# Performance work log

Hardware: AMD Instinct MI355X
Metric: run time of the kernel (lower is better)

## Reference

```python
import jax, jax.numpy as jnp
import numpy as np

HEADS = 8
DIM_HEAD = 64
SCALE = DIM_HEAD ** -0.5


def setup_inputs() -> dict:
    key = jax.random.key(0)
    k1, k2, k3, k4 = jax.random.split(key, 4)
    b, n, dim = 4, 1024, 512
    inner = HEADS * DIM_HEAD  # 512
    x = jax.random.normal(k1, (b, n, dim), dtype=jnp.float32)
    spd = jax.random.normal(k2, (b, HEADS, n, n), dtype=jnp.float32)
    head_keep = jnp.ones((HEADS,), dtype=jnp.float32)  # deterministic stand-in for binomial head drop
    w_qkv = jax.random.normal(k3, (dim, 3 * inner), dtype=jnp.float32) * (dim ** -0.5)
    w_out = jax.random.normal(k4, (inner, dim), dtype=jnp.float32) * (inner ** -0.5)
    b_out = jnp.zeros((dim,), dtype=jnp.float32)
    return {"x": x, "spd": spd, "head_keep": head_keep, "w_qkv": w_qkv, "w_out": w_out, "b_out": b_out}


def reference(x, spd, head_keep, w_qkv, w_out, b_out):
    b, n, dim = x.shape
    qkv = x @ w_qkv  # [b, n, 3*inner]
    q, k, v = jnp.split(qkv, 3, axis=-1)

    def to_heads(t):  # [b, n, h*d] -> [b, h, n, d]
        return t.reshape(b, n, HEADS, DIM_HEAD).transpose(0, 2, 1, 3)

    q, k, v = to_heads(q), to_heads(k), to_heads(v)
    dots = jnp.einsum('bhid,bhjd->bhij', q, k) * SCALE + spd  # [b, h, n, n]
    attn = jax.nn.softmax(dots, axis=-1)
    # random head drop + rescale: attn * mask * H / sum(keep)
    keep_sum = jnp.sum(head_keep)
    attn = attn * (head_keep[None, :, None, None] * (HEADS / keep_sum))
    out = jnp.einsum('bhij,bhjd->bhid', attn, v)  # [b, h, n, d]
    out = out.transpose(0, 2, 1, 3).reshape(b, n, HEADS * DIM_HEAD)
    return out @ w_out + b_out
```

## Files before the change

### kernel.cpp

```cpp
#include <hip/hip_runtime.h>
#include <math.h>

#define NSEQ   1024
#define HEADS  8
#define DHEAD  64
#define SCALE  0.125f
#define LOG2E  1.4426950408889634f

typedef unsigned int u32;
typedef unsigned short u16;
typedef short short8 __attribute__((ext_vector_type(8)));
typedef __bf16 bf16x2 __attribute__((ext_vector_type(2)));
typedef __bf16 bf16x8 __attribute__((ext_vector_type(8)));
typedef float f32x4  __attribute__((ext_vector_type(4)));
typedef float f32x16 __attribute__((ext_vector_type(16)));

__device__ __forceinline__ u16 f2bf(float f) {
    __bf16 h = (__bf16)f;
    return __builtin_bit_cast(u16, h);
}
__device__ __forceinline__ u32 pk2(float lo, float hi) {
    bf16x2 v; v[0] = (__bf16)lo; v[1] = (__bf16)hi;
    return __builtin_bit_cast(u32, v);
}
__device__ __forceinline__ float exp2_fast(float x) {
#if __has_builtin(__builtin_amdgcn_exp2f)
    return __builtin_amdgcn_exp2f(x);
#else
    return exp2f(x);
#endif
}
__device__ __forceinline__ f32x4 mfma16(short8 a, short8 b, f32x4 c) {
    return __builtin_amdgcn_mfma_f32_16x16x32_bf16(a, b, c, 0, 0, 0);
}
__device__ __forceinline__ f32x16 mfma32(short8 a, short8 b, f32x16 c) {
    return __builtin_amdgcn_mfma_f32_32x32x16_bf16(a, b, c, 0, 0, 0);
}

__global__ __launch_bounds__(256) void prep(const float* __restrict__ x,
                                            const float* __restrict__ wqkv,
                                            const float* __restrict__ wout,
                                            u16* __restrict__ x_bf,
                                            u16* __restrict__ wqkvT,
                                            u16* __restrict__ woutT) {
    __shared__ float T[64][65];
    const int t = threadIdx.x;
    const int bb = blockIdx.x;
    if (bb < 1024) {
        int i = (bb * 256 + t) * 8;
        float4 a = *(const float4*)&x[i];
        float4 b = *(const float4*)&x[i + 4];
        bf16x8 v;
        v[0] = (__bf16)a.x; v[1] = (__bf16)a.y; v[2] = (__bf16)a.z; v[3] = (__bf16)a.w;
        v[4] = (__bf16)b.x; v[5] = (__bf16)b.y; v[6] = (__bf16)b.z; v[7] = (__bf16)b.w;
        *(short8*)&x_bf[i] = __builtin_bit_cast(short8, v);
        return;
    }
    const float* in; u16* outp; int K, N, n0, k0;
    if (bb < 1216) {
        int bid = bb - 1024;
        in = wqkv; outp = wqkvT; K = 512; N = 1536;
        n0 = (bid % 24) * 64; k0 = (bid / 24) * 64;
    } else {
        int bid = bb - 1216;
        in = wout; outp = woutT; K = 512; N = 512;
        n0 = (bid % 8) * 64; k0 = (bid / 8) * 64;
    }
    #pragma unroll
    for (int rep = 0; rep < 4; ++rep) {
        int r = rep * 16 + (t >> 4), c = (t & 15) * 4;
        float4 v = *(const float4*)&in[(size_t)(k0 + r) * N + n0 + c];
        T[r][c + 0] = v.x; T[r][c + 1] = v.y; T[r][c + 2] = v.z; T[r][c + 3] = v.w;
    }
    __syncthreads();
    const int nl = t >> 2, kb = (t & 3) * 16;
    bf16x8 s0, s1;
    #pragma unroll
    for (int e = 0; e < 8; ++e) s0[e] = (__bf16)T[kb + e][nl];
    #pragma unroll
    for (int e = 0; e < 8; ++e) s1[e] = (__bf16)T[kb + 8 + e][nl];
    *(short8*)&outp[(size_t)(n0 + nl) * K + k0 + kb]     = __builtin_bit_cast(short8, s0);
    *(short8*)&outp[(size_t)(n0 + nl) * K + k0 + kb + 8] = __builtin_bit_cast(short8, s1);
}

__global__ __launch_bounds__(256) void gemm_qkv_mfma(const u16* __restrict__ xb,
                                                     const u16* __restrict__ wT,
                                                     u16* __restrict__ qb,
                                                     u16* __restrict__ kb,
                                                     u16* __restrict__ vT) {
    __shared__ u16 As[128][40];
    __shared__ u16 Bs[64][40];
    const int t = threadIdx.x, lane = t & 63, w = t >> 6;
    const int wm = w >> 1, wn = w & 1;
    const int l15 = lane & 15, l4 = lane >> 4;
    const int j0 = blockIdx.x * 64, i0 = blockIdx.y * 128;
    const int which = j0 / 512;
    const int b = i0 >> 10;

    f32x4 acc[8];
    #pragma unroll
    for (int i = 0; i < 8; ++i) acc[i] = (f32x4){0.f, 0.f, 0.f, 0.f};

    short8 ra[2], rbv;
    #pragma unroll
    for (int rep = 0; rep < 2; ++rep) {
        int row = rep * 64 + (t >> 2), c8 = (t & 3) * 8;
        ra[rep] = *(const short8*)&xb[(size_t)(i0 + row) * 512 + c8];
    }
    {
        int row = t >> 2, c8 = (t & 3) * 8;
        rbv = *(const short8*)&wT[(size_t)(j0 + row) * 512 + c8];
    }

    for (int kt = 0; kt < 16; ++kt) {
        __syncthreads();
        #pragma unroll
        for (int rep = 0; rep < 2; ++rep) {
            int row = rep * 64 + (t >> 2), c8 = (t & 3) * 8;
            *(short8*)&As[row][c8] = ra[rep];
        }
        {
            int row = t >> 2, c8 = (t & 3) * 8;
            *(short8*)&Bs[row][c8] = rbv;
        }
        __syncthreads();
        if (kt < 15) {
            int k0 = (kt + 1) * 32;
            #pragma unroll
            for (int rep = 0; rep < 2; ++rep) {
                int row = rep * 64 + (t >> 2), c8 = (t & 3) * 8;
                ra[rep] = *(const short8*)&xb[(size_t)(i0 + row) * 512 + k0 + c8];
            }
            int row = t >> 2, c8 = (t & 3) * 8;
            rbv = *(const short8*)&wT[(size_t)(j0 + row) * 512 + k0 + c8];
        }
        if (which < 2) {
            short8 af[4], bf[2];
            #pragma unroll
            for (int m = 0; m < 4; ++m)
                af[m] = *(const short8*)&As[wm * 64 + m * 16 + l15][l4 * 8];
            #pragma unroll
            for (int n = 0; n < 2; ++n)
                bf[n] = *(const short8*)&Bs[wn * 32 + n * 16 + l15][l4 * 8];
            #pragma unroll
            for (int m = 0; m < 4; ++m)
                #pragma unroll
                for (int n = 0; n < 2; ++n)
                    acc[m * 2 + n] = mfma16(af[m], bf[n], acc[m * 2 + n]);
        } else {
            short8 af[2], bf[4];
            #pragma unroll
            for (int mj = 0; mj < 2; ++mj)
                af[mj] = *(const short8*)&Bs[wn * 32 + mj * 16 + l15][l4 * 8];
            #pragma unroll
            for (int ni = 0; ni < 4; ++ni)
                bf[ni] = *(const short8*)&As[wm * 64 + ni * 16 + l15][l4 * 8];
            #pragma unroll
            for (int mj = 0; mj < 2; ++mj)
                #pragma unroll
                for (int ni = 0; ni < 4; ++ni)
                    acc[mj * 4 + ni] = mfma16(af[mj], bf[ni], acc[mj * 4 + ni]);
        }
    }

    if (which < 2) {
        u16* dst = (which == 0) ? qb : kb;
        const int h = (j0 & 511) >> 6;
        #pragma unroll
        for (int m = 0; m < 4; ++m)
            #pragma unroll
            for (int n = 0; n < 2; ++n) {
                int d = wn * 32 + n * 16 + l15;
                #pragma unroll
                for (int r = 0; r < 4; ++r) {
                    int tok = i0 + wm * 64 + m * 16 + l4 * 4 + r;
                    dst[(((size_t)(b * HEADS + h)) * NSEQ + (tok & 1023)) * DHEAD + d] =
                        f2bf(acc[m * 2 + n][r]);
                }
            }
    } else {
        const int h = (j0 - 1024) >> 6;
        #pragma unroll
        for (int mj = 0; mj < 2; ++mj)
            #pragma unroll
            for (int ni = 0; ni < 4; ++ni) {
                int tok = i0 + wm * 64 + ni * 16 + l15;
                #pragma unroll
                for (int r = 0; r < 4; ++r) {
                    int d = wn * 32 + mj * 16 + l4 * 4 + r;
                    vT[(((size_t)(b * HEADS + h)) * DHEAD + d) * NSEQ + (tok & 1023)] =
                        f2bf(acc[mj * 4 + ni][r]);
                }
            }
    }
}

__global__ __launch_bounds__(256) void attn_mfma(const u16* __restrict__ qb,
                                                 const u16* __restrict__ kb,
                                                 const u16* __restrict__ vT,
                                                 const float* __restrict__ spd,
                                                 const float* __restrict__ head_keep,
                                                 u16* __restrict__ ab) {
    __shared__ u16 Qs[128][72];
    __shared__ u16 Ks[64][72];
    __shared__ u16 Vs[64][72];
    __shared__ float Ss[128][65];

    const int t = threadIdx.x, lane = t & 63, w = t >> 6;
    const int hi = lane >> 5, li = lane & 31;
    const int bh = blockIdx.y, b = bh >> 3, h = bh & 7;
    const int i0 = blockIdx.x * 128;

    const u16* qh = qb + (size_t)bh * NSEQ * DHEAD;
    const u16* kh = kb + (size_t)bh * NSEQ * DHEAD;
    const u16* vh = vT + (size_t)bh * DHEAD * NSEQ;
    const float* sp = spd + (size_t)bh * NSEQ * NSEQ;

    #pragma unroll
    for (int rep = 0; rep < 4; ++rep) {
        int row = rep * 32 + (t >> 3), c8 = (t & 7) * 8;
        *(short8*)&Qs[row][c8] = *(const short8*)&qh[(size_t)(i0 + row) * DHEAD + c8];
    }

    float m_s = -1e30f, l_s = 0.f;
    f32x16 o0 = {}, o1 = {};
    #pragma unroll
    for (int r = 0; r < 16; ++r) { o0[r] = 0.f; o1[r] = 0.f; }

    short8 rk[2], rv[2];
    float4 rs[8];
    {
        int row = t >> 3, c8 = (t & 7) * 8;
        #pragma unroll
        for (int rep = 0; rep < 2; ++rep) {
            rk[rep] = *(const short8*)&kh[(size_t)(rep * 32 + row) * DHEAD + c8];
            rv[rep] = *(const short8*)&vh[(size_t)(rep * 32 + row) * NSEQ + c8];
        }
        #pragma unroll
        for (int rep = 0; rep < 8; ++rep) {
            int rrow = rep * 16 + (t >> 4), c = (t & 15) * 4;
            rs[rep] = *(const float4*)&sp[(size_t)(i0 + rrow) * NSEQ + c];
        }
    }

    for (int jt = 0; jt < 16; ++jt) {
        __syncthreads();
        {
            int row = t >> 3, c8 = (t & 7) * 8;
            #pragma unroll
            for (int rep = 0; rep < 2; ++rep) {
                *(short8*)&Ks[rep * 32 + row][c8] = rk[rep];
                *(short8*)&Vs[rep * 32 + row][c8] = rv[rep];
            }
            #pragma unroll
            for (int rep = 0; rep < 8; ++rep) {
                int rrow = rep * 16 + (t >> 4), c = (t & 15) * 4;
                Ss[rrow][c + 0] = rs[rep].x * LOG2E;
                Ss[rrow][c + 1] = rs[rep].y * LOG2E;
                Ss[rrow][c + 2] = rs[rep].z * LOG2E;
                Ss[rrow][c + 3] = rs[rep].w * LOG2E;
            }
        }
        __syncthreads();
        if (jt < 15) {
            int j0n = (jt + 1) * 64;
            int row = t >> 3, c8 = (t & 7) * 8;
            #pragma unroll
            for (int rep = 0; rep < 2; ++rep) {
                rk[rep] = *(const short8*)&kh[(size_t)(j0n + rep * 32 + row) * DHEAD + c8];
                rv[rep] = *(const short8*)&vh[(size_t)(rep * 32 + row) * NSEQ + j0n + c8];
            }
            #pragma unroll
            for (int rep = 0; rep < 8; ++rep) {
                int rrow = rep * 16 + (t >> 4), c = (t & 15) * 4;
                rs[rep] = *(const float4*)&sp[(size_t)(i0 + rrow) * NSEQ + j0n + c];
            }
        }

        f32x16 s2[2];
        #pragma unroll
        for (int kg = 0; kg < 2; ++kg) {
            #pragma unroll
            for (int r = 0; r < 16; ++r) s2[kg][r] = 0.f;
            #pragma unroll
            for (int ds = 0; ds < 4; ++ds) {
                short8 ak = *(const short8*)&Ks[kg * 32 + li][ds * 16 + hi * 8];
                short8 bq = *(const short8*)&Qs[w * 32 + li][ds * 16 + hi * 8];
                s2[kg] = mfma32(ak, bq, s2[kg]);
            }
        }

        float p2[32];
        #pragma unroll
        for (int kg = 0; kg < 2; ++kg)
            #pragma unroll
            for (int r = 0; r < 16; ++r) {
                int key = kg * 32 + (r & 3) + 8 * (r >> 2) + 4 * hi;
                p2[kg * 16 + r] = fmaf(s2[kg][r], SCALE * LOG2E, Ss[w * 32 + li][key]);
            }
        float m16[16];
        #pragma unroll
        for (int r = 0; r < 16; ++r) m16[r] = fmaxf(p2[r], p2[r + 16]);
        float m8v[8];
        #pragma unroll
        for (int r = 0; r < 8; ++r) m8v[r] = fmaxf(m16[r], m16[r + 8]);
        float m4v[4];
        #pragma unroll
        for (int r = 0; r < 4; ++r) m4v[r] = fmaxf(m8v[r], m8v[r + 4]);
        float pmax = fmaxf(fmaxf(m4v[0], m4v[1]), fmaxf(m4v[2], m4v[3]));
        pmax = fmaxf(pmax, __shfl_xor(pmax, 32));

        if (!__all(pmax <= m_s + 12.0f)) {
            float mnew = fmaxf(m_s, pmax);
            float fac = exp2_fast(m_s - mnew);
            m_s = mnew;
            l_s *= fac;
            #pragma unroll
            for (int r = 0; r < 16; ++r) {
                int ip = (r & 3) + 8 * (r >> 2) + 4 * hi;
                float fr = __shfl(fac, ip);
                o0[r] *= fr; o1[r] *= fr;
            }
        }

        float p[32];
        float sa0 = 0.f, sa1 = 0.f, sa2 = 0.f, sa3 = 0.f;
        #pragma unroll
        for (int r = 0; r < 32; r += 4) {
            p[r + 0] = exp2_fast(p2[r + 0] - m_s); sa0 += p[r + 0];
            p[r + 1] = exp2_fast(p2[r + 1] - m_s); sa1 += p[r + 1];
            p[r + 2] = exp2_fast(p2[r + 2] - m_s); sa2 += p[r + 2];
            p[r + 3] = exp2_fast(p2[r + 3] - m_s); sa3 += p[r + 3];
        }
        float rsum = (sa0 + sa1) + (sa2 + sa3);
        rsum += __shfl_xor(rsum, 32);
        l_s += rsum;

        short8 pf[4];
        #pragma unroll
        for (int ks = 0; ks < 4; ++ks) {
            int rb = (ks >> 1) * 16 + (ks & 1) * 8;
            u32 a0 = pk2(p[rb + 0], p[rb + 1]);
            u32 a1 = pk2(p[rb + 2], p[rb + 3]);
            u32 a2 = pk2(p[rb + 4], p[rb + 5]);
            u32 a3 = pk2(p[rb + 6], p[rb + 7]);
            u32 x0 = (u32)__shfl_xor((int)a0, 32);
            u32 x1 = (u32)__shfl_xor((int)a1, 32);
            u32 x2 = (u32)__shfl_xor((int)a2, 32);
            u32 x3 = (u32)__shfl_xor((int)a3, 32);
            union { u32 u[4]; short8 v; } c4;
            c4.u[0] = hi ? x2 : a0;
            c4.u[1] = hi ? x3 : a1;
            c4.u[2] = hi ? a2 : x0;
            c4.u[3] = hi ? a3 : x1;
            pf[ks] = c4.v;
        }

        #pragma unroll
        for (int ks = 0; ks < 4; ++ks) {
            short8 v0f = *(const short8*)&Vs[li][ks * 16 + hi * 8];
            short8 v1f = *(const short8*)&Vs[32 + li][ks * 16 + hi * 8];
            o0 = mfma32(pf[ks], v0f, o0);
            o1 = mfma32(pf[ks], v1f, o1);
        }
    }

    float ksum = 0.f;
    #pragma unroll
    for (int i = 0; i < HEADS; ++i) ksum += head_keep[i];
    const float hscale = head_keep[h] * (float)HEADS / ksum;
    const float inv = hscale / l_s;
    #pragma unroll
    for (int r = 0; r < 16; ++r) {
        int ip = (r & 3) + 8 * (r >> 2) + 4 * hi;
        float invr = __shfl(inv, ip);
        int tok = i0 + w * 32 + ip;
        size_t base = ((size_t)(b * NSEQ) + tok) * 512 + h * DHEAD;
        ab[base + li]      = f2bf(o0[r] * invr);
        ab[base + 32 + li] = f2bf(o1[r] * invr);
    }
}

__global__ __launch_bounds__(256) void gemm_out_mfma(const u16* __restrict__ abuf,
                                                     const u16* __restrict__ wT,
                                                     const float* __restrict__ bias,
                                                     float* __restrict__ out) {
    __shared__ u16 As[64][40];
    __shared__ u16 Bs[64][40];
    const int t = threadIdx.x, lane = t & 63, w = t >> 6;
    const int wm = w >> 1, wn = w & 1;
    const int l15 = lane & 15, l4 = lane >> 4;
    const int j0 = blockIdx.x * 64, i0 = blockIdx.y * 64;

    f32x4 acc[2][2];
    #pragma unroll
    for (int m = 0; m < 2; ++m)
        #pragma unroll
        for (int n = 0; n < 2; ++n) acc[m][n] = (f32x4){0.f, 0.f, 0.f, 0.f};

    short8 rav, rbv;
    {
        int row = t >> 2, c8 = (t & 3) * 8;
        rav = *(const short8*)&abuf[(size_t)(i0 + row) * 512 + c8];
        rbv = *(const short8*)&wT[(size_t)(j0 + row) * 512 + c8];
    }

    for (int kt = 0; kt < 16; ++kt) {
        __syncthreads();
        {
            int row = t >> 2, c8 = (t & 3) * 8;
            *(short8*)&As[row][c8] = rav;
            *(short8*)&Bs[row][c8] = rbv;
        }
        __syncthreads();
        if (kt < 15) {
            int k0 = (kt + 1) * 32;
            int row = t >> 2, c8 = (t & 3) * 8;
            rav = *(const short8*)&abuf[(size_t)(i0 + row) * 512 + k0 + c8];
            rbv = *(const short8*)&wT[(size_t)(j0 + row) * 512 + k0 + c8];
        }
        short8 af[2], bf[2];
        #pragma unroll
        for (int m = 0; m < 2; ++m)
            af[m] = *(const short8*)&As[wm * 32 + m * 16 + l15][l4 * 8];
        #pragma unroll
        for (int n = 0; n < 2; ++n)
            bf[n] = *(const short8*)&Bs[wn * 32 + n * 16 + l15][l4 * 8];
        #pragma unroll
        for (int m = 0; m < 2; ++m)
            #pragma unroll
            for (int n = 0; n < 2; ++n)
                acc[m][n] = mfma16(af[m], bf[n], acc[m][n]);
    }

    #pragma unroll
    for (int m = 0; m < 2; ++m)
        #pragma unroll
        for (int n = 0; n < 2; ++n) {
            int col = j0 + wn * 32 + n * 16 + l15;
            float bb = bias[col];
            #pragma unroll
            for (int r = 0; r < 4; ++r) {
                int row = i0 + wm * 32 + m * 16 + l4 * 4 + r;
                out[(size_t)row * 512 + col] = acc[m][n][r] + bb;
            }
        }
}

extern "C" void kernel_launch(void* const* d_in, const int* in_sizes, int n_in,
                              void* d_out, int out_size, void* d_ws, size_t ws_size,
                              hipStream_t stream) {
    const float* x         = (const float*)d_in[0];
    const float* spd       = (const float*)d_in[1];
    const float* head_keep = (const float*)d_in[2];
    const float* w_qkv     = (const float*)d_in[3];
    const float* w_out     = (const float*)d_in[4];
    const float* b_out     = (const float*)d_in[5];
    float* out = (float*)d_out;

    char* ws = (char*)d_ws;
    u16* x_bf   = (u16*)(ws);
    u16* wqkvT  = (u16*)(ws + (4u << 20));
    u16* woutT  = (u16*)(ws + (4u << 20) + 1572864);
    u16* qb     = (u16*)(ws + (6u << 20));
    u16* kb     = (u16*)(ws + (10u << 20));
    u16* vT     = (u16*)(ws + (14u << 20));
    u16* ab     = (u16*)(ws + (18u << 20));

    prep<<<1280, 256, 0, stream>>>(x, w_qkv, w_out, x_bf, wqkvT, woutT);
    gemm_qkv_mfma<<<dim3(24, 32), 256, 0, stream>>>(x_bf, wqkvT, qb, kb, vT);
    attn_mfma<<<dim3(8, 32), 256, 0, stream>>>(qb, kb, vT, spd, head_keep, ab);
    gemm_out_mfma<<<dim3(8, 64), 256, 0, stream>>>(ab, woutT, b_out, out);
}
```

Measured before the change: 67.60 us.

## Fuse x bf16 conversion into QKV GEMM, widen K-tiles, swizzle block order

```diff
diff --git a/kernel.cpp b/kernel.cpp
--- a/kernel.cpp
+++ b/kernel.cpp
@@ -23,6 +23,12 @@
     bf16x2 v; v[0] = (__bf16)lo; v[1] = (__bf16)hi;
     return __builtin_bit_cast(u32, v);
 }
+__device__ __forceinline__ short8 cvt8(float4 a, float4 b) {
+    bf16x8 v;
+    v[0] = (__bf16)a.x; v[1] = (__bf16)a.y; v[2] = (__bf16)a.z; v[3] = (__bf16)a.w;
+    v[4] = (__bf16)b.x; v[5] = (__bf16)b.y; v[6] = (__bf16)b.z; v[7] = (__bf16)b.w;
+    return __builtin_bit_cast(short8, v);
+}
 __device__ __forceinline__ float exp2_fast(float x) {
 #if __has_builtin(__builtin_amdgcn_exp2f)
     return __builtin_amdgcn_exp2f(x);
@@ -37,32 +43,19 @@
     return __builtin_amdgcn_mfma_f32_32x32x16_bf16(a, b, c, 0, 0, 0);
 }
 
-__global__ __launch_bounds__(256) void prep(const float* __restrict__ x,
-                                            const float* __restrict__ wqkv,
+__global__ __launch_bounds__(256) void prep(const float* __restrict__ wqkv,
                                             const float* __restrict__ wout,
-                                            u16* __restrict__ x_bf,
                                             u16* __restrict__ wqkvT,
                                             u16* __restrict__ woutT) {
     __shared__ float T[64][65];
     const int t = threadIdx.x;
     const int bb = blockIdx.x;
-    if (bb < 1024) {
-        int i = (bb * 256 + t) * 8;
-        float4 a = *(const float4*)&x[i];
-        float4 b = *(const float4*)&x[i + 4];
-        bf16x8 v;
-        v[0] = (__bf16)a.x; v[1] = (__bf16)a.y; v[2] = (__bf16)a.z; v[3] = (__bf16)a.w;
-        v[4] = (__bf16)b.x; v[5] = (__bf16)b.y; v[6] = (__bf16)b.z; v[7] = (__bf16)b.w;
-        *(short8*)&x_bf[i] = __builtin_bit_cast(short8, v);
-        return;
-    }
     const float* in; u16* outp; int K, N, n0, k0;
-    if (bb < 1216) {
-        int bid = bb - 1024;
+    if (bb < 192) {
         in = wqkv; outp = wqkvT; K = 512; N = 1536;
-        n0 = (bid % 24) * 64; k0 = (bid / 24) * 64;
+        n0 = (bb % 24) * 64; k0 = (bb / 24) * 64;
     } else {
-        int bid = bb - 1216;
+        int bid = bb - 192;
         in = wout; outp = woutT; K = 512; N = 512;
         n0 = (bid % 8) * 64; k0 = (bid / 8) * 64;
     }
@@ -83,17 +76,19 @@
     *(short8*)&outp[(size_t)(n0 + nl) * K + k0 + kb + 8] = __builtin_bit_cast(short8, s1);
 }
 
-__global__ __launch_bounds__(256) void gemm_qkv_mfma(const u16* __restrict__ xb,
+__global__ __launch_bounds__(256) void gemm_qkv_mfma(const float* __restrict__ x,
                                                      const u16* __restrict__ wT,
                                                      u16* __restrict__ qb,
                                                      u16* __restrict__ kb,
                                                      u16* __restrict__ vT) {
-    __shared__ u16 As[128][40];
-    __shared__ u16 Bs[64][40];
+    __shared__ u16 As[128][72];
+    __shared__ u16 Bs[64][72];
     const int t = threadIdx.x, lane = t & 63, w = t >> 6;
     const int wm = w >> 1, wn = w & 1;
     const int l15 = lane & 15, l4 = lane >> 4;
-    const int j0 = blockIdx.x * 64, i0 = blockIdx.y * 128;
+    const int bid = blockIdx.x;
+    const int swz = (bid & 7) * 96 + (bid >> 3);
+    const int j0 = (swz % 24) * 64, i0 = (swz / 24) * 128;
     const int which = j0 / 512;
     const int b = i0 >> 10;
 
@@ -101,65 +96,69 @@
     #pragma unroll
     for (int i = 0; i < 8; ++i) acc[i] = (f32x4){0.f, 0.f, 0.f, 0.f};
 
-    short8 ra[2], rbv;
-    #pragma unroll
-    for (int rep = 0; rep < 2; ++rep) {
-        int row = rep * 64 + (t >> 2), c8 = (t & 3) * 8;
-        ra[rep] = *(const short8*)&xb[(size_t)(i0 + row) * 512 + c8];
-    }
-    {
-        int row = t >> 2, c8 = (t & 3) * 8;
-        rbv = *(const short8*)&wT[(size_t)(j0 + row) * 512 + c8];
-    }
-
-    for (int kt = 0; kt < 16; ++kt) {
+    const int arow0 = t >> 2, c16 = (t & 3) * 16;
+
+    float4 rax[8];
+    short8 rb2[2];
+    #pragma unroll
+    for (int rep = 0; rep < 2; ++rep)
+        #pragma unroll
+        for (int q = 0; q < 4; ++q)
+            rax[rep * 4 + q] = *(const float4*)&x[(size_t)(i0 + rep * 64 + arow0) * 512 + c16 + q * 4];
+    #pragma unroll
+    for (int q = 0; q < 2; ++q)
+        rb2[q] = *(const short8*)&wT[(size_t)(j0 + arow0) * 512 + c16 + q * 8];
+
+    for (int kt = 0; kt < 8; ++kt) {
         __syncthreads();
         #pragma unroll
         for (int rep = 0; rep < 2; ++rep) {
-            int row = rep * 64 + (t >> 2), c8 = (t & 3) * 8;
-            *(short8*)&As[row][c8] = ra[rep];
-        }
-        {
-            int row = t >> 2, c8 = (t & 3) * 8;
-            *(short8*)&Bs[row][c8] = rbv;
-        }
-        __syncthreads();
-        if (kt < 15) {
-            int k0 = (kt + 1) * 32;
-            #pragma unroll
-            for (int rep = 0; rep < 2; ++rep) {
-                int row = rep * 64 + (t >> 2), c8 = (t & 3) * 8;
-                ra[rep] = *(const short8*)&xb[(size_t)(i0 + row) * 512 + k0 + c8];
-            }
-            int row = t >> 2, c8 = (t & 3) * 8;
-            rbv = *(const short8*)&wT[(size_t)(j0 + row) * 512 + k0 + c8];
-        }
-        if (which < 2) {
-            short8 af[4], bf[2];
-            #pragma unroll
-            for (int m = 0; m < 4; ++m)
-                af[m] = *(const short8*)&As[wm * 64 + m * 16 + l15][l4 * 8];
-            #pragma unroll
-            for (int n = 0; n < 2; ++n)
-                bf[n] = *(const short8*)&Bs[wn * 32 + n * 16 + l15][l4 * 8];
-            #pragma unroll
-            for (int m = 0; m < 4; ++m)
+            *(short8*)&As[rep * 64 + arow0][c16]     = cvt8(rax[rep * 4 + 0], rax[rep * 4 + 1]);
+            *(short8*)&As[rep * 64 + arow0][c16 + 8] = cvt8(rax[rep * 4 + 2], rax[rep * 4 + 3]);
+        }
+        *(short8*)&Bs[arow0][c16]     = rb2[0];
+        *(short8*)&Bs[arow0][c16 + 8] = rb2[1];
+        __syncthreads();
+        if (kt < 7) {
+            int k0 = (kt + 1) * 64;
+            #pragma unroll
+            for (int rep = 0; rep < 2; ++rep)
+                #pragma unroll
+                for (int q = 0; q < 4; ++q)
+                    rax[rep * 4 + q] = *(const float4*)&x[(size_t)(i0 + rep * 64 + arow0) * 512 + k0 + c16 + q * 4];
+            #pragma unroll
+            for (int q = 0; q < 2; ++q)
+                rb2[q] = *(const short8*)&wT[(size_t)(j0 + arow0) * 512 + k0 + c16 + q * 8];
+        }
+        #pragma unroll
+        for (int ks = 0; ks < 2; ++ks) {
+            if (which < 2) {
+                short8 af[4], bf[2];
+                #pragma unroll
+                for (int m = 0; m < 4; ++m)
+                    af[m] = *(const short8*)&As[wm * 64 + m * 16 + l15][ks * 32 + l4 * 8];
                 #pragma unroll
                 for (int n = 0; n < 2; ++n)
-                    acc[m * 2 + n] = mfma16(af[m], bf[n], acc[m * 2 + n]);
-        } else {
-            short8 af[2], bf[4];
-            #pragma unroll
-            for (int mj = 0; mj < 2; ++mj)
-                af[mj] = *(const short8*)&Bs[wn * 32 + mj * 16 + l15][l4 * 8];
-            #pragma unroll
-            for (int ni = 0; ni < 4; ++ni)
-                bf[ni] = *(const short8*)&As[wm * 64 + ni * 16 + l15][l4 * 8];
-            #pragma unroll
-            for (int mj = 0; mj < 2; ++mj)
+                    bf[n] = *(const short8*)&Bs[wn * 32 + n * 16 + l15][ks * 32 + l4 * 8];
+                #pragma unroll
+                for (int m = 0; m < 4; ++m)
+                    #pragma unroll
+                    for (int n = 0; n < 2; ++n)
+                        acc[m * 2 + n] = mfma16(af[m], bf[n], acc[m * 2 + n]);
+            } else {
+                short8 af[2], bf[4];
+                #pragma unroll
+                for (int mj = 0; mj < 2; ++mj)
+                    af[mj] = *(const short8*)&Bs[wn * 32 + mj * 16 + l15][ks * 32 + l4 * 8];
                 #pragma unroll
                 for (int ni = 0; ni < 4; ++ni)
-                    acc[mj * 4 + ni] = mfma16(af[mj], bf[ni], acc[mj * 4 + ni]);
+                    bf[ni] = *(const short8*)&As[wm * 64 + ni * 16 + l15][ks * 32 + l4 * 8];
+                #pragma unroll
+                for (int mj = 0; mj < 2; ++mj)
+                    #pragma unroll
+                    for (int ni = 0; ni < 4; ++ni)
+                        acc[mj * 4 + ni] = mfma16(af[mj], bf[ni], acc[mj * 4 + ni]);
+            }
         }
     }
 
@@ -385,12 +384,14 @@
                                                      const u16* __restrict__ wT,
                                                      const float* __restrict__ bias,
                                                      float* __restrict__ out) {
-    __shared__ u16 As[64][40];
-    __shared__ u16 Bs[64][40];
+    __shared__ u16 As[64][72];
+    __shared__ u16 Bs[64][72];
     const int t = threadIdx.x, lane = t & 63, w = t >> 6;
     const int wm = w >> 1, wn = w & 1;
     const int l15 = lane & 15, l4 = lane >> 4;
-    const int j0 = blockIdx.x * 64, i0 = blockIdx.y * 64;
+    const int bid = blockIdx.x;
+    const int swz = (bid & 7) * 64 + (bid >> 3);
+    const int j0 = (swz % 8) * 64, i0 = (swz / 8) * 64;
 
     f32x4 acc[2][2];
     #pragma unroll
@@ -398,39 +399,45 @@
         #pragma unroll
         for (int n = 0; n < 2; ++n) acc[m][n] = (f32x4){0.f, 0.f, 0.f, 0.f};
 
-    short8 rav, rbv;
-    {
-        int row = t >> 2, c8 = (t & 3) * 8;
-        rav = *(const short8*)&abuf[(size_t)(i0 + row) * 512 + c8];
-        rbv = *(const short8*)&wT[(size_t)(j0 + row) * 512 + c8];
-    }
-
-    for (int kt = 0; kt < 16; ++kt) {
-        __syncthreads();
-        {
-            int row = t >> 2, c8 = (t & 3) * 8;
-            *(short8*)&As[row][c8] = rav;
-            *(short8*)&Bs[row][c8] = rbv;
-        }
-        __syncthreads();
-        if (kt < 15) {
-            int k0 = (kt + 1) * 32;
-            int row = t >> 2, c8 = (t & 3) * 8;
-            rav = *(const short8*)&abuf[(size_t)(i0 + row) * 512 + k0 + c8];
-            rbv = *(const short8*)&wT[(size_t)(j0 + row) * 512 + k0 + c8];
-        }
-        short8 af[2], bf[2];
-        #pragma unroll
-        for (int m = 0; m < 2; ++m)
-            af[m] = *(const short8*)&As[wm * 32 + m * 16 + l15][l4 * 8];
-        #pragma unroll
-        for (int n = 0; n < 2; ++n)
-            bf[n] = *(const short8*)&Bs[wn * 32 + n * 16 + l15][l4 * 8];
-        #pragma unroll
-        for (int m = 0; m < 2; ++m)
+    const int row0 = t >> 2, c16 = (t & 3) * 16;
+    short8 rav[2], rbv[2];
+    #pragma unroll
+    for (int q = 0; q < 2; ++q) {
+        rav[q] = *(const short8*)&abuf[(size_t)(i0 + row0) * 512 + c16 + q * 8];
+        rbv[q] = *(const short8*)&wT[(size_t)(j0 + row0) * 512 + c16 + q * 8];
+    }
+
+    for (int kt = 0; kt < 8; ++kt) {
+        __syncthreads();
+        #pragma unroll
+        for (int q = 0; q < 2; ++q) {
+            *(short8*)&As[row0][c16 + q * 8] = rav[q];
+            *(short8*)&Bs[row0][c16 + q * 8] = rbv[q];
+        }
+        __syncthreads();
+        if (kt < 7) {
+            int k0 = (kt + 1) * 64;
+            #pragma unroll
+            for (int q = 0; q < 2; ++q) {
+                rav[q] = *(const short8*)&abuf[(size_t)(i0 + row0) * 512 + k0 + c16 + q * 8];
+                rbv[q] = *(const short8*)&wT[(size_t)(j0 + row0) * 512 + k0 + c16 + q * 8];
+            }
+        }
+        #pragma unroll
+        for (int ks = 0; ks < 2; ++ks) {
+            short8 af[2], bf[2];
+            #pragma unroll
+            for (int m = 0; m < 2; ++m)
+                af[m] = *(const short8*)&As[wm * 32 + m * 16 + l15][ks * 32 + l4 * 8];
             #pragma unroll
             for (int n = 0; n < 2; ++n)
-                acc[m][n] = mfma16(af[m], bf[n], acc[m][n]);
+                bf[n] = *(const short8*)&Bs[wn * 32 + n * 16 + l15][ks * 32 + l4 * 8];
+            #pragma unroll
+            for (int m = 0; m < 2; ++m)
+                #pragma unroll
+                for (int n = 0; n < 2; ++n)
+                    acc[m][n] = mfma16(af[m], bf[n], acc[m][n]);
+        }
     }
 
     #pragma unroll
@@ -459,7 +466,6 @@
     float* out = (float*)d_out;
 
     char* ws = (char*)d_ws;
-    u16* x_bf   = (u16*)(ws);
     u16* wqkvT  = (u16*)(ws + (4u << 20));
     u16* woutT  = (u16*)(ws + (4u << 20) + 1572864);
     u16* qb     = (u16*)(ws + (6u << 20));
@@ -467,8 +473,8 @@
     u16* vT     = (u16*)(ws + (14u << 20));
     u16* ab     = (u16*)(ws + (18u << 20));
 
-    prep<<<1280, 256, 0, stream>>>(x, w_qkv, w_out, x_bf, wqkvT, woutT);
-    gemm_qkv_mfma<<<dim3(24, 32), 256, 0, stream>>>(x_bf, wqkvT, qb, kb, vT);
+    prep<<<256, 256, 0, stream>>>(w_qkv, w_out, wqkvT, woutT);
+    gemm_qkv_mfma<<<768, 256, 0, stream>>>(x, wqkvT, qb, kb, vT);
     attn_mfma<<<dim3(8, 32), 256, 0, stream>>>(qb, kb, vT, spd, head_keep, ab);
-    gemm_out_mfma<<<dim3(8, 64), 256, 0, stream>>>(ab, woutT, b_out, out);
-}
+    gemm_out_mfma<<<512, 256, 0, stream>>>(ab, woutT, b_out, out);
+}
```

After: 69.36 us. 2.6% more time.

## Double-buffer K/V/bias tiles in LDS to drop one barrier per iteration

Applied to the files above, without the earlier changes.

```diff
diff --git a/kernel.cpp b/kernel.cpp
--- a/kernel.cpp
+++ b/kernel.cpp
@@ -202,9 +202,9 @@
                                                  const float* __restrict__ head_keep,
                                                  u16* __restrict__ ab) {
     __shared__ u16 Qs[128][72];
-    __shared__ u16 Ks[64][72];
-    __shared__ u16 Vs[64][72];
-    __shared__ float Ss[128][65];
+    __shared__ u16 Kd[2][64][72];
+    __shared__ u16 Vd[2][64][72];
+    __shared__ float Sd[2][128][65];
 
     const int t = threadIdx.x, lane = t & 63, w = t >> 6;
     const int hi = lane >> 5, li = lane & 31;
@@ -222,60 +222,49 @@
         *(short8*)&Qs[row][c8] = *(const short8*)&qh[(size_t)(i0 + row) * DHEAD + c8];
     }
 
+    const int krow = t >> 3, kc8 = (t & 7) * 8;
+    const int srow = t >> 4, sc = (t & 15) * 4;
+
+    short8 rk[2], rv[2];
+    float4 rs[8];
+    #pragma unroll
+    for (int rep = 0; rep < 2; ++rep) {
+        rk[rep] = *(const short8*)&kh[(size_t)(rep * 32 + krow) * DHEAD + kc8];
+        rv[rep] = *(const short8*)&vh[(size_t)(rep * 32 + krow) * NSEQ + kc8];
+    }
+    #pragma unroll
+    for (int rep = 0; rep < 8; ++rep)
+        rs[rep] = *(const float4*)&sp[(size_t)(i0 + rep * 16 + srow) * NSEQ + sc];
+    #pragma unroll
+    for (int rep = 0; rep < 2; ++rep) {
+        *(short8*)&Kd[0][rep * 32 + krow][kc8] = rk[rep];
+        *(short8*)&Vd[0][rep * 32 + krow][kc8] = rv[rep];
+    }
+    #pragma unroll
+    for (int rep = 0; rep < 8; ++rep) {
+        int rrow = rep * 16 + srow;
+        Sd[0][rrow][sc + 0] = rs[rep].x * LOG2E;
+        Sd[0][rrow][sc + 1] = rs[rep].y * LOG2E;
+        Sd[0][rrow][sc + 2] = rs[rep].z * LOG2E;
+        Sd[0][rrow][sc + 3] = rs[rep].w * LOG2E;
+    }
+    #pragma unroll
+    for (int rep = 0; rep < 2; ++rep) {
+        rk[rep] = *(const short8*)&kh[(size_t)(64 + rep * 32 + krow) * DHEAD + kc8];
+        rv[rep] = *(const short8*)&vh[(size_t)(rep * 32 + krow) * NSEQ + 64 + kc8];
+    }
+    #pragma unroll
+    for (int rep = 0; rep < 8; ++rep)
+        rs[rep] = *(const float4*)&sp[(size_t)(i0 + rep * 16 + srow) * NSEQ + 64 + sc];
+    __syncthreads();
+
     float m_s = -1e30f, l_s = 0.f;
     f32x16 o0 = {}, o1 = {};
     #pragma unroll
     for (int r = 0; r < 16; ++r) { o0[r] = 0.f; o1[r] = 0.f; }
 
-    short8 rk[2], rv[2];
-    float4 rs[8];
-    {
-        int row = t >> 3, c8 = (t & 7) * 8;
-        #pragma unroll
-        for (int rep = 0; rep < 2; ++rep) {
-            rk[rep] = *(const short8*)&kh[(size_t)(rep * 32 + row) * DHEAD + c8];
-            rv[rep] = *(const short8*)&vh[(size_t)(rep * 32 + row) * NSEQ + c8];
-        }
-        #pragma unroll
-        for (int rep = 0; rep < 8; ++rep) {
-            int rrow = rep * 16 + (t >> 4), c = (t & 15) * 4;
-            rs[rep] = *(const float4*)&sp[(size_t)(i0 + rrow) * NSEQ + c];
-        }
-    }
-
     for (int jt = 0; jt < 16; ++jt) {
-        __syncthreads();
-        {
-            int row = t >> 3, c8 = (t & 7) * 8;
-            #pragma unroll
-            for (int rep = 0; rep < 2; ++rep) {
-                *(short8*)&Ks[rep * 32 + row][c8] = rk[rep];
-                *(short8*)&Vs[rep * 32 + row][c8] = rv[rep];
-            }
-            #pragma unroll
-            for (int rep = 0; rep < 8; ++rep) {
-                int rrow = rep * 16 + (t >> 4), c = (t & 15) * 4;
-                Ss[rrow][c + 0] = rs[rep].x * LOG2E;
-                Ss[rrow][c + 1] = rs[rep].y * LOG2E;
-                Ss[rrow][c + 2] = rs[rep].z * LOG2E;
-                Ss[rrow][c + 3] = rs[rep].w * LOG2E;
-            }
-        }
-        __syncthreads();
-        if (jt < 15) {
-            int j0n = (jt + 1) * 64;
-            int row = t >> 3, c8 = (t & 7) * 8;
-            #pragma unroll
-            for (int rep = 0; rep < 2; ++rep) {
-                rk[rep] = *(const short8*)&kh[(size_t)(j0n + rep * 32 + row) * DHEAD + c8];
-                rv[rep] = *(const short8*)&vh[(size_t)(rep * 32 + row) * NSEQ + j0n + c8];
-            }
-            #pragma unroll
-            for (int rep = 0; rep < 8; ++rep) {
-                int rrow = rep * 16 + (t >> 4), c = (t & 15) * 4;
-                rs[rep] = *(const float4*)&sp[(size_t)(i0 + rrow) * NSEQ + j0n + c];
-            }
-        }
+        const int cur = jt & 1;
 
         f32x16 s2[2];
         #pragma unroll
@@ -284,7 +273,7 @@
             for (int r = 0; r < 16; ++r) s2[kg][r] = 0.f;
             #pragma unroll
             for (int ds = 0; ds < 4; ++ds) {
-                short8 ak = *(const short8*)&Ks[kg * 32 + li][ds * 16 + hi * 8];
+                short8 ak = *(const short8*)&Kd[cur][kg * 32 + li][ds * 16 + hi * 8];
                 short8 bq = *(const short8*)&Qs[w * 32 + li][ds * 16 + hi * 8];
                 s2[kg] = mfma32(ak, bq, s2[kg]);
             }
@@ -296,7 +285,7 @@
             #pragma unroll
             for (int r = 0; r < 16; ++r) {
                 int key = kg * 32 + (r & 3) + 8 * (r >> 2) + 4 * hi;
-                p2[kg * 16 + r] = fmaf(s2[kg][r], SCALE * LOG2E, Ss[w * 32 + li][key]);
+                p2[kg * 16 + r] = fmaf(s2[kg][r], SCALE * LOG2E, Sd[cur][w * 32 + li][key]);
             }
         float m16[16];
         #pragma unroll
@@ -358,10 +347,39 @@
 
         #pragma unroll
         for (int ks = 0; ks < 4; ++ks) {
-            short8 v0f = *(const short8*)&Vs[li][ks * 16 + hi * 8];
-            short8 v1f = *(const short8*)&Vs[32 + li][ks * 16 + hi * 8];
+            short8 v0f = *(const short8*)&Vd[cur][li][ks * 16 + hi * 8];
+            short8 v1f = *(const short8*)&Vd[cur][32 + li][ks * 16 + hi * 8];
             o0 = mfma32(pf[ks], v0f, o0);
             o1 = mfma32(pf[ks], v1f, o1);
+        }
+
+        if (jt < 15) {
+            const int nxt = cur ^ 1;
+            #pragma unroll
+            for (int rep = 0; rep < 2; ++rep) {
+                *(short8*)&Kd[nxt][rep * 32 + krow][kc8] = rk[rep];
+                *(short8*)&Vd[nxt][rep * 32 + krow][kc8] = rv[rep];
+            }
+            #pragma unroll
+            for (int rep = 0; rep < 8; ++rep) {
+                int rrow = rep * 16 + srow;
+                Sd[nxt][rrow][sc + 0] = rs[rep].x * LOG2E;
+                Sd[nxt][rrow][sc + 1] = rs[rep].y * LOG2E;
+                Sd[nxt][rrow][sc + 2] = rs[rep].z * LOG2E;
+                Sd[nxt][rrow][sc + 3] = rs[rep].w * LOG2E;
+            }
+            if (jt < 14) {
+                int j0n = (jt + 2) * 64;
+                #pragma unroll
+                for (int rep = 0; rep < 2; ++rep) {
+                    rk[rep] = *(const short8*)&kh[(size_t)(j0n + rep * 32 + krow) * DHEAD + kc8];
+                    rv[rep] = *(const short8*)&vh[(size_t)(rep * 32 + krow) * NSEQ + j0n + kc8];
+                }
+                #pragma unroll
+                for (int rep = 0; rep < 8; ++rep)
+                    rs[rep] = *(const float4*)&sp[(size_t)(i0 + rep * 16 + srow) * NSEQ + j0n + sc];
+            }
+            __syncthreads();
         }
     }
 
```

New measurement: 66.35 us. Within noise of the previous version (-1.8%).
